# Kernel optimization log

Measured on AMD Instinct MI355X. Metric: run time of the kernel, lower is better.

Reference implementation:

```python
import jax, jax.numpy as jnp
import numpy as np

B, D_MODEL, N_LAYERS = 8, 512, 4
D_STATE, D_CONV, EXPAND, DT_RANK = 16, 4, 2, 32
D_INNER = EXPAND * D_MODEL
NUM_CLASSES = 10
ALPHA = 0.2  # observer_alpha
LN_EPS = 1e-5


def setup_inputs() -> dict:
    key = jax.random.key(0)
    ks = jax.random.split(key, 10)
    std = 0.02
    rn = lambda k, sh: (jax.random.normal(k, sh) * std).astype(jnp.float32)
    return {
        "x": jax.random.normal(ks[0], (B, 3, 32, 32), dtype=jnp.float32),
        "W_inp": rn(ks[1], (3, D_MODEL)), "b_inp": jnp.zeros((D_MODEL,), jnp.float32),
        "W_in": rn(ks[2], (N_LAYERS, D_MODEL, 2 * D_INNER)), "b_in": jnp.zeros((N_LAYERS, 2 * D_INNER), jnp.float32),
        "conv_w": rn(ks[3], (N_LAYERS, D_INNER, D_CONV)), "conv_b": jnp.zeros((N_LAYERS, D_INNER), jnp.float32),
        "W_x": rn(ks[4], (N_LAYERS, D_INNER, DT_RANK + 2 * D_STATE)),
        "W_dt": rn(ks[5], (N_LAYERS, DT_RANK, D_INNER)), "b_dt": jnp.zeros((N_LAYERS, D_INNER), jnp.float32),
        "A_log": jnp.broadcast_to(jnp.log(jnp.arange(1, D_STATE + 1, dtype=jnp.float32)), (N_LAYERS, D_INNER, D_STATE)) + 0.0,
        "D_skip": jnp.ones((N_LAYERS, D_INNER), jnp.float32),
        "W_out": rn(ks[6], (N_LAYERS, D_INNER, D_MODEL)), "b_out": jnp.zeros((N_LAYERS, D_MODEL), jnp.float32),
        "ln_w": jnp.ones((N_LAYERS, D_MODEL), jnp.float32), "ln_b": jnp.zeros((N_LAYERS, D_MODEL), jnp.float32),
        "lnf_w": jnp.ones((D_MODEL,), jnp.float32), "lnf_b": jnp.zeros((D_MODEL,), jnp.float32),
        "W_cls": rn(ks[7], (D_MODEL, NUM_CLASSES)), "b_cls": jnp.zeros((NUM_CLASSES,), jnp.float32),
    }


def layernorm(x, w, b):
    mu = x.mean(-1, keepdims=True)
    var = jnp.mean(jnp.square(x - mu), -1, keepdims=True)
    return (x - mu) * jax.lax.rsqrt(var + LN_EPS) * w + b


def mamba_layer(x, Wi, bi, cw, cb, Wx, Wdt, bdt, Alog, Dv, Wo, bo):
    # x: [B, L, d_model]
    Bsz, L, _ = x.shape
    u, z = jnp.split(x @ Wi + bi, 2, axis=-1)  # each [B, L, d_inner]
    # causal depthwise conv1d, kernel width D_CONV
    up = jnp.pad(u, ((0, 0), (D_CONV - 1, 0), (0, 0)))
    uc = cb + sum(up[:, k:k + L, :] * cw[:, k] for k in range(D_CONV))
    uc = jax.nn.silu(uc)
    dbc = uc @ Wx  # [B, L, dt_rank + 2*d_state]
    dt = jax.nn.softplus(dbc[..., :DT_RANK] @ Wdt + bdt)       # [B, L, d_inner]
    Bm = dbc[..., DT_RANK:DT_RANK + D_STATE]                    # [B, L, d_state]
    Cm = dbc[..., DT_RANK + D_STATE:]                           # [B, L, d_state]
    A = -jnp.exp(Alog)                                          # [d_inner, d_state]

    def step(h, inp):
        u_t, dt_t, B_t, C_t = inp  # [B,E],[B,E],[B,N],[B,N]
        h = jnp.exp(dt_t[..., None] * A) * h + (dt_t * u_t)[..., None] * B_t[:, None, :]
        # Luenberger observer correction: h <- h + alpha * (u - C.h) * C^T
        err = u_t - jnp.einsum('ben,bn->be', h, C_t)
        h = h + ALPHA * err[..., None] * C_t[:, None, :]
        y = jnp.einsum('ben,bn->be', h, C_t)
        return h, y

    step = jax.checkpoint(step)
    h0 = jnp.zeros((Bsz, D_INNER, D_STATE), dtype=x.dtype)
    xs = (uc.transpose(1, 0, 2), dt.transpose(1, 0, 2), Bm.transpose(1, 0, 2), Cm.transpose(1, 0, 2))
    _, ys = jax.lax.scan(step, h0, xs)
    y = ys.transpose(1, 0, 2) + Dv * uc
    y = y * jax.nn.silu(z)
    return y @ Wo + bo


def reference(x, W_inp, b_inp, W_in, b_in, conv_w, conv_b, W_x, W_dt, b_dt, A_log, D_skip, W_out, b_out, ln_w, ln_b, lnf_w, lnf_b, W_cls, b_cls):
    Bsz = x.shape[0]
    t = x.transpose(0, 2, 3, 1).reshape(Bsz, -1, 3)  # [B, H*W, 3]
    t = t @ W_inp + b_inp                             # [B, L, d_model]
    for i in range(N_LAYERS):
        t = t + mamba_layer(layernorm(t, ln_w[i], ln_b[i]), W_in[i], b_in[i], conv_w[i], conv_b[i], W_x[i], W_dt[i], b_dt[i], A_log[i], D_skip[i], W_out[i], b_out[i])
    t = t.mean(axis=1)
    t = layernorm(t, lnf_w, lnf_b)
    return t @ W_cls + b_cls
```

## Files before the change

kernel.cpp:

```cpp
#include <hip/hip_runtime.h>
#include <hip/hip_bf16.h>
#include <math.h>

#define BSZ 8
#define SEQL 1024
#define DM 512
#define DI 1024
#define DST 16
#define DTR 32
#define NLAYERS 4
#define ALPHA_C 0.2f
#define LNEPS 1e-5f
#define CH 64
#define KS64 8
#define YSTR 18

typedef __attribute__((ext_vector_type(8))) short short8;
typedef __attribute__((ext_vector_type(4))) float f32x4;

__device__ __forceinline__ void gll16(const void* g, void* l) {
    __builtin_amdgcn_global_load_lds(
        (const __attribute__((address_space(1))) unsigned int*)g,
        (__attribute__((address_space(3))) unsigned int*)l, 16, 0, 0);
}

__device__ __forceinline__ float sum16(float x) {
    x += __int_as_float(__builtin_amdgcn_update_dpp(0, __float_as_int(x), 0x121, 0xf, 0xf, true));
    x += __int_as_float(__builtin_amdgcn_update_dpp(0, __float_as_int(x), 0x122, 0xf, 0xf, true));
    x += __int_as_float(__builtin_amdgcn_update_dpp(0, __float_as_int(x), 0x124, 0xf, 0xf, true));
    x += __int_as_float(__builtin_amdgcn_update_dpp(0, __float_as_int(x), 0x128, 0xf, 0xf, true));
    return x;
}

__device__ __forceinline__ float bf2f(unsigned short v) {
    return __uint_as_float(((unsigned)v) << 16);
}

__global__ __launch_bounds__(256) void embed_kernel(const float* __restrict__ x,
                                                    const float* __restrict__ Wi,
                                                    const float* __restrict__ bi,
                                                    float* __restrict__ t) {
    int idx = blockIdx.x * 256 + threadIdx.x;
    if (idx >= BSZ * SEQL * DM) return;
    int d  = idx & (DM - 1);
    int bl = idx >> 9;
    int l  = bl & (SEQL - 1);
    int b  = bl >> 10;
    const float* xb = x + (size_t)b * 3 * SEQL;
    float acc = bi[d];
    acc += xb[0 * SEQL + l] * Wi[0 * DM + d];
    acc += xb[1 * SEQL + l] * Wi[1 * DM + d];
    acc += xb[2 * SEQL + l] * Wi[2 * DM + d];
    t[idx] = acc;
}

__global__ __launch_bounds__(256) void ln_kernel(const float* __restrict__ t,
                                                 const float* __restrict__ w,
                                                 const float* __restrict__ b,
                                                 __hip_bfloat16* __restrict__ xn) {
    int row = blockIdx.x;
    int tid = threadIdx.x;
    const float* r = t + (size_t)row * DM;
    float v0 = r[tid], v1 = r[tid + 256];
    __shared__ float sh[256], sh2[256];
    sh[tid]  = v0 + v1;
    sh2[tid] = v0 * v0 + v1 * v1;
    __syncthreads();
    for (int off = 128; off > 0; off >>= 1) {
        if (tid < off) { sh[tid] += sh[tid + off]; sh2[tid] += sh2[tid + off]; }
        __syncthreads();
    }
    float mu  = sh[0]  * (1.f / DM);
    float var = sh2[0] * (1.f / DM) - mu * mu;
    float rs  = rsqrtf(var + LNEPS);
    xn[(size_t)row * DM + tid]       = __float2bfloat16((v0 - mu) * rs * w[tid]       + b[tid]);
    xn[(size_t)row * DM + tid + 256] = __float2bfloat16((v1 - mu) * rs * w[tid + 256] + b[tid + 256]);
}

__global__ __launch_bounds__(256) void transpose_bf_kernel(const float* __restrict__ W,
                                                           __hip_bfloat16* __restrict__ Wt,
                                                           int K, int N, size_t lstride) {
    const float* Wl = W + (size_t)blockIdx.z * lstride;
    __hip_bfloat16* Wtl = Wt + (size_t)blockIdx.z * lstride;
    __shared__ float tile[32][33];
    int kk = blockIdx.x * 32, nn = blockIdx.y * 32;
    int tx = threadIdx.x & 31, ty = threadIdx.x >> 5;
#pragma unroll
    for (int i = 0; i < 32; i += 8)
        tile[ty + i][tx] = Wl[(size_t)(kk + ty + i) * N + nn + tx];
    __syncthreads();
#pragma unroll
    for (int i = 0; i < 32; i += 8)
        Wtl[(size_t)(nn + ty + i) * K + kk + tx] = __float2bfloat16(tile[tx][ty + i]);
}

template <int OUTMODE>
__global__ __launch_bounds__(256) void gemm_mfma_kernel(const short* __restrict__ A,
                                                        const short* __restrict__ Bt,
                                                        const float* __restrict__ bias,
                                                        void* __restrict__ Cv,
                                                        int M, int N, int K) {
    __shared__ __align__(16) short As[128 * 32];
    __shared__ __align__(16) short Bs[128 * 32];
    int tid = threadIdx.x;
    int w = tid >> 6, lane = tid & 63;
    int quad = lane >> 4, ml = lane & 15;
    int wm = w & 1, wn = w >> 1;
    const short* Ab = A + (size_t)blockIdx.x * 128 * K;
    const short* Bb = Bt + (size_t)blockIdx.y * 128 * K;
    f32x4 acc[4][4] = {};
    int s0 = tid, s1 = tid + 256;
    int r0 = s0 >> 2, c0 = (s0 & 3) ^ ((r0 >> 1) & 3);
    int r1 = s1 >> 2, c1 = (s1 & 3) ^ ((r1 >> 1) & 3);
    int aoff[4], boff[4];
#pragma unroll
    for (int t = 0; t < 4; t++) {
        int ra = wm * 64 + t * 16 + ml;
        aoff[t] = ra * 32 + (quad ^ ((ra >> 1) & 3)) * 8;
        int rb = wn * 64 + t * 16 + ml;
        boff[t] = rb * 32 + (quad ^ ((rb >> 1) & 3)) * 8;
    }
    for (int kk = 0; kk < K; kk += 32) {
        gll16(Ab + (size_t)r0 * K + kk + c0 * 8, As + (size_t)(w * 64) * 8);
        gll16(Ab + (size_t)r1 * K + kk + c1 * 8, As + (size_t)(256 + w * 64) * 8);
        gll16(Bb + (size_t)r0 * K + kk + c0 * 8, Bs + (size_t)(w * 64) * 8);
        gll16(Bb + (size_t)r1 * K + kk + c1 * 8, Bs + (size_t)(256 + w * 64) * 8);
        __syncthreads();
        short8 af[4], bfr[4];
#pragma unroll
        for (int t = 0; t < 4; t++) af[t]  = *(const short8*)&As[aoff[t]];
#pragma unroll
        for (int t = 0; t < 4; t++) bfr[t] = *(const short8*)&Bs[boff[t]];
#pragma unroll
        for (int mt = 0; mt < 4; mt++)
#pragma unroll
            for (int nt = 0; nt < 4; nt++)
                acc[mt][nt] = __builtin_amdgcn_mfma_f32_16x16x32_bf16(af[mt], bfr[nt], acc[mt][nt], 0, 0, 0);
        __syncthreads();
    }
#pragma unroll
    for (int mt = 0; mt < 4; mt++) {
#pragma unroll
        for (int nt = 0; nt < 4; nt++) {
            int n = blockIdx.y * 128 + wn * 64 + nt * 16 + ml;
            float bv = bias[n];
#pragma unroll
            for (int r = 0; r < 4; r++) {
                int m = blockIdx.x * 128 + wm * 64 + mt * 16 + quad * 4 + r;
                size_t off = (size_t)m * N + n;
                float v = acc[mt][nt][r] + bv;
                if (OUTMODE == 2) {
                    ((unsigned short*)Cv)[off] = __bfloat16_as_ushort(__float2bfloat16(v));
                } else {
                    float* C = (float*)Cv;
                    if (OUTMODE == 1) v += C[off];
                    C[off] = v;
                }
            }
        }
    }
}

__global__ __launch_bounds__(256) void gemm6464_res_kernel(const short* __restrict__ A,
                                                           const short* __restrict__ Bt,
                                                           const float* __restrict__ bias,
                                                           float* __restrict__ C,
                                                           int M, int N, int K) {
    __shared__ __align__(16) short As[64 * 32];
    __shared__ __align__(16) short Bs[64 * 32];
    int tid = threadIdx.x;
    int w = tid >> 6, lane = tid & 63;
    int quad = lane >> 4, ml = lane & 15;
    int wm = w & 1, wn = w >> 1;
    const short* Ab = A + (size_t)blockIdx.x * 64 * K;
    const short* Bb = Bt + (size_t)blockIdx.y * 64 * K;
    f32x4 acc[2][2] = {};
    int r0 = tid >> 2, c0 = (tid & 3) ^ ((r0 >> 1) & 3);
    int aoff[2], boff[2];
#pragma unroll
    for (int t = 0; t < 2; t++) {
        int ra = wm * 32 + t * 16 + ml;
        aoff[t] = ra * 32 + (quad ^ ((ra >> 1) & 3)) * 8;
        int rb = wn * 32 + t * 16 + ml;
        boff[t] = rb * 32 + (quad ^ ((rb >> 1) & 3)) * 8;
    }
    for (int kk = 0; kk < K; kk += 32) {
        gll16(Ab + (size_t)r0 * K + kk + c0 * 8, As + (size_t)(w * 64) * 8);
        gll16(Bb + (size_t)r0 * K + kk + c0 * 8, Bs + (size_t)(w * 64) * 8);
        __syncthreads();
        short8 af[2], bfr[2];
#pragma unroll
        for (int t = 0; t < 2; t++) af[t]  = *(const short8*)&As[aoff[t]];
#pragma unroll
        for (int t = 0; t < 2; t++) bfr[t] = *(const short8*)&Bs[boff[t]];
#pragma unroll
        for (int mt = 0; mt < 2; mt++)
#pragma unroll
            for (int nt = 0; nt < 2; nt++)
                acc[mt][nt] = __builtin_amdgcn_mfma_f32_16x16x32_bf16(af[mt], bfr[nt], acc[mt][nt], 0, 0, 0);
        __syncthreads();
    }
#pragma unroll
    for (int mt = 0; mt < 2; mt++) {
#pragma unroll
        for (int nt = 0; nt < 2; nt++) {
            int n = blockIdx.y * 64 + wn * 32 + nt * 16 + ml;
            float bv = bias[n];
#pragma unroll
            for (int r = 0; r < 4; r++) {
                int m = blockIdx.x * 64 + wm * 32 + mt * 16 + quad * 4 + r;
                size_t off = (size_t)m * N + n;
                C[off] = acc[mt][nt][r] + bv + C[off];
            }
        }
    }
}

__global__ __launch_bounds__(256) void conv_kernel(const unsigned short* __restrict__ uzb,
                                                   const float* __restrict__ cw,
                                                   const float* __restrict__ cb,
                                                   unsigned short* __restrict__ ucb) {
    int idx = blockIdx.x * 256 + threadIdx.x;
    int e  = idx & (DI - 1);
    int bl = idx >> 10;
    int l  = bl & (SEQL - 1);
    int b  = bl >> 10;
    const unsigned short* u = uzb + (size_t)b * SEQL * 2048;
    float acc = cb[e];
#pragma unroll
    for (int k = 0; k < 4; k++) {
        int ll = l - 3 + k;
        float uv = (ll >= 0) ? bf2f(u[(size_t)ll * 2048 + e]) : 0.f;
        acc += uv * cw[e * 4 + k];
    }
    acc = acc / (1.f + __expf(-acc));
    ucb[idx] = __bfloat16_as_ushort(__float2bfloat16(acc));
}

__global__ __launch_bounds__(256) void gemm64_mfma_kernel(const short* __restrict__ A,
                                                          const short* __restrict__ Bt,
                                                          float* __restrict__ part,
                                                          int M) {
    const int K = DI;
    const int Kseg = K / KS64;
    __shared__ __align__(16) short As[128 * 32];
    __shared__ __align__(16) short Bs[64 * 32];
    int tid = threadIdx.x;
    int w = tid >> 6, lane = tid & 63;
    int quad = lane >> 4, ml = lane & 15;
    int wm = w & 1, wn = w >> 1;
    int bm = blockIdx.x, ks = blockIdx.y;
    const short* Ab = A + (size_t)bm * 128 * K;
    f32x4 acc[4][2] = {};
    int s0 = tid, s1 = tid + 256;
    int r0 = s0 >> 2, c0 = (s0 & 3) ^ ((r0 >> 1) & 3);
    int r1 = s1 >> 2, c1 = (s1 & 3) ^ ((r1 >> 1) & 3);
    int rB = tid >> 2, cB = (tid & 3) ^ ((rB >> 1) & 3);
    int aoff[4], boff[2];
#pragma unroll
    for (int t = 0; t < 4; t++) {
        int ra = wm * 64 + t * 16 + ml;
        aoff[t] = ra * 32 + (quad ^ ((ra >> 1) & 3)) * 8;
    }
#pragma unroll
    for (int t = 0; t < 2; t++) {
        int rb = wn * 32 + t * 16 + ml;
        boff[t] = rb * 32 + (quad ^ ((rb >> 1) & 3)) * 8;
    }
    int k0 = ks * Kseg;
    for (int kk = k0; kk < k0 + Kseg; kk += 32) {
        gll16(Ab + (size_t)r0 * K + kk + c0 * 8, As + (size_t)(w * 64) * 8);
        gll16(Ab + (size_t)r1 * K + kk + c1 * 8, As + (size_t)(256 + w * 64) * 8);
        gll16(Bt + (size_t)rB * K + kk + cB * 8, Bs + (size_t)(w * 64) * 8);
        __syncthreads();
        short8 af[4], bfr[2];
#pragma unroll
        for (int t = 0; t < 4; t++) af[t]  = *(const short8*)&As[aoff[t]];
#pragma unroll
        for (int t = 0; t < 2; t++) bfr[t] = *(const short8*)&Bs[boff[t]];
#pragma unroll
        for (int mt = 0; mt < 4; mt++)
#pragma unroll
            for (int nt = 0; nt < 2; nt++)
                acc[mt][nt] = __builtin_amdgcn_mfma_f32_16x16x32_bf16(af[mt], bfr[nt], acc[mt][nt], 0, 0, 0);
        __syncthreads();
    }
#pragma unroll
    for (int mt = 0; mt < 4; mt++) {
#pragma unroll
        for (int nt = 0; nt < 2; nt++) {
            int n = wn * 32 + nt * 16 + ml;
#pragma unroll
            for (int r = 0; r < 4; r++) {
                int m = bm * 128 + wm * 64 + mt * 16 + quad * 4 + r;
                part[((size_t)ks * M + m) * 64 + n] = acc[mt][nt][r];
            }
        }
    }
}

__global__ __launch_bounds__(256) void repack_kernel(const float* __restrict__ part,
                                                     unsigned* __restrict__ bcb,
                                                     float* __restrict__ ssqb,
                                                     int M) {
    int m = blockIdx.x * 8 + (threadIdx.x >> 5);
    int j = threadIdx.x & 31;
    float v = 0.f;
#pragma unroll
    for (int ks = 0; ks < KS64; ks++) v += part[((size_t)ks * M + m) * 64 + 32 + j];
    int n = j & 15;
    unsigned short u16 = __bfloat16_as_ushort(__float2bfloat16(v));
    unsigned short* bp = (unsigned short*)(bcb + (size_t)m * 16 + n);
    if (j < 16) {
        bp[0] = u16;
    } else {
        bp[1] = u16;
        float vr = bf2f(u16);
        float s = sum16(vr * vr);
        if (j == 16) ssqb[m] = s;
    }
}

__global__ __launch_bounds__(256) void dt_kernel(const float* __restrict__ part,
                                                 const float* __restrict__ Wdt,
                                                 const float* __restrict__ bdt,
                                                 const unsigned short* __restrict__ ucb,
                                                 unsigned* __restrict__ dub,
                                                 int M) {
    __shared__ float sdtc[32][32];
    __shared__ float swdt[32][256];
    int tid = threadIdx.x;
    int e0 = (blockIdx.x & 3) * 256;
    int m0 = (blockIdx.x >> 2) * 32;
#pragma unroll
    for (int i = 0; i < 4; i++) {
        int idx = tid + 256 * i;
        int m = idx >> 5, r = idx & 31;
        float v = 0.f;
#pragma unroll
        for (int ks = 0; ks < KS64; ks++) v += part[((size_t)ks * M + m0 + m) * 64 + r];
        sdtc[m][r] = v;
    }
#pragma unroll
    for (int r = 0; r < 32; r++) swdt[r][tid] = Wdt[(size_t)r * DI + e0 + tid];
    __syncthreads();
    float wc[32];
#pragma unroll
    for (int r = 0; r < 32; r++) wc[r] = swdt[r][tid];
    float bv = bdt[e0 + tid];
    for (int m = 0; m < 32; m++) {
        float acc = bv;
#pragma unroll
        for (int r4 = 0; r4 < 8; r4++) {
            float4 d4 = *(const float4*)&sdtc[m][r4 * 4];
            acc = fmaf(d4.x, wc[r4 * 4 + 0], acc);
            acc = fmaf(d4.y, wc[r4 * 4 + 1], acc);
            acc = fmaf(d4.z, wc[r4 * 4 + 2], acc);
            acc = fmaf(d4.w, wc[r4 * 4 + 3], acc);
        }
        float sp = (acc > 20.f) ? acc : log1pf(__expf(acc));
        unsigned dt16 = (unsigned)__bfloat16_as_ushort(__float2bfloat16(sp));
        unsigned u16  = (unsigned)ucb[(size_t)(m0 + m) * DI + e0 + tid];
        dub[(size_t)(m0 + m) * DI + e0 + tid] = (dt16 << 16) | u16;
    }
}

__device__ __forceinline__ void scan_stage(unsigned* sDU, unsigned* sBC,
                                           const unsigned* __restrict__ dub_row,
                                           const unsigned* __restrict__ bcb_row,
                                           int e_base, int tid, int tc) {
    int w = tid >> 6;
    int t4 = tid >> 2, c4 = tid & 3;
    gll16(dub_row + (size_t)(tc + t4) * 1024 + e_base + c4 * 4, sDU + w * 256);
    gll16(bcb_row + (size_t)(tc + t4) * 16 + c4 * 4,            sBC + w * 256);
}

__device__ __forceinline__ void scan_flush(const float* yb, __hip_bfloat16* ob,
                                           int e_base, int tcp, int tid) {
#pragma unroll
    for (int r = 0; r < 2; r++) {
        int pid = r * 256 + tid;
        int t = pid >> 3, ep = pid & 7;
        float2 y2 = *(const float2*)&yb[t * YSTR + ep * 2];
        __hip_bfloat162 v;
        v.x = __float2bfloat16(y2.x);
        v.y = __float2bfloat16(y2.y);
        *(__hip_bfloat162*)&ob[(size_t)(tcp + t) * DI + e_base + ep * 2] = v;
    }
}

__global__ __launch_bounds__(256) void scan_kernel(const unsigned* __restrict__ dub,
                                                   const unsigned short* __restrict__ uzb,
                                                   const unsigned* __restrict__ bcb,
                                                   const float* __restrict__ ssqb,
                                                   const float* __restrict__ Alog,
                                                   const float* __restrict__ Dv,
                                                   __hip_bfloat16* __restrict__ out) {
    __shared__ __align__(16) unsigned sDU[2][CH * 16];
    __shared__ __align__(16) unsigned sBC[2][CH * 16];
    __shared__ __align__(16) float    yb [2][CH * YSTR];
    int tid = threadIdx.x;
    int g = tid >> 4, n = tid & 15;
    int b = blockIdx.x >> 6;
    int e_base = (blockIdx.x & 63) << 4;
    int e = e_base + g;
    float An2 = -__expf(Alog[e * DST + n]) * 1.4426950408889634f;
    float dv = Dv[e];
    const unsigned*       dub_row = dub + (size_t)b * SEQL * DI;
    const unsigned short* uzb_row = uzb + (size_t)b * SEQL * 2048;
    const unsigned*       bcb_row = bcb + (size_t)b * SEQL * 16;
    const float*          sqb     = ssqb + (size_t)b * SEQL;
    __hip_bfloat16* ob = out + (size_t)b * SEQL * DI;
    float h = 0.f;
    scan_stage(sDU[0], sBC[0], dub_row, bcb_row, e_base, tid, 0);
    int buf = 0;
    for (int c = 0; c < SEQL / CH; c++) {
        int tc = c * CH;
        __syncthreads();
        if (c + 1 < SEQL / CH)
            scan_stage(sDU[buf ^ 1], sBC[buf ^ 1], dub_row, bcb_row, e_base, tid, tc + CH);
        if (c > 0)
            scan_flush(yb[buf ^ 1], ob, e_base, tc - CH, tid);
        const unsigned* pDU = sDU[buf];
        const unsigned* pBC = sBC[buf];
        float* pY = yb[buf];
        for (int ts = 0; ts < CH; ts += 16) {
            int tl = ts + n;
            float sq = sqb[tc + tl];
            float zv = bf2f(uzb_row[(size_t)(tc + tl) * 2048 + 1024 + e]);
            float pc = 0.f, ucap = 0.f;
#pragma unroll
            for (int j = 0; j < 16; j++) {
                int t = ts + j;
                unsigned du = pDU[t * 16 + g];
                float dtv = __uint_as_float(du & 0xFFFF0000u);
                float uv  = __uint_as_float(du << 16);
                unsigned bcd = pBC[t * 16 + n];
                float Bn = __uint_as_float(bcd << 16);
                float Cn = __uint_as_float(bcd & 0xFFFF0000u);
                float a = __builtin_amdgcn_exp2f(dtv * An2);
                h = fmaf(a, h, dtv * uv * Bn);
                float p = sum16(h * Cn);
                h = fmaf(uv - p, ALPHA_C * Cn, h);
                bool cap = (n == j);
                pc   = cap ? p  : pc;
                ucap = cap ? uv : ucap;
            }
            float es2 = ALPHA_C * (ucap - pc);
            float y = fmaf(dv, ucap, fmaf(es2, sq, pc));
            float sz = zv / (1.f + __expf(-zv));
            pY[tl * YSTR + g] = y * sz;
        }
        buf ^= 1;
    }
    __syncthreads();
    scan_flush(yb[buf ^ 1], ob, e_base, SEQL - CH, tid);
}

__global__ __launch_bounds__(512) void pool_kernel(const float* __restrict__ t,
                                                   float* __restrict__ part) {
    int b = blockIdx.x >> 4;
    int c = blockIdx.x & 15;
    int d = threadIdx.x;
    const float* tb = t + ((size_t)b * SEQL + c * 64) * DM + d;
    float s = 0.f;
    for (int l = 0; l < 64; l++) s += tb[(size_t)l * DM];
    part[(size_t)blockIdx.x * DM + d] = s;
}

__global__ __launch_bounds__(512) void final_kernel(const float* __restrict__ part,
                                                    const float* __restrict__ lw,
                                                    const float* __restrict__ lb,
                                                    const float* __restrict__ Wc,
                                                    const float* __restrict__ bc,
                                                    float* __restrict__ out) {
    int b = blockIdx.x;
    int d = threadIdx.x;
    float v = 0.f;
    for (int c = 0; c < 16; c++) v += part[((size_t)b * 16 + c) * DM + d];
    v *= (1.f / SEQL);
    __shared__ float sh[512], sh2[512], nd[512];
    sh[d] = v; sh2[d] = v * v;
    __syncthreads();
    for (int off = 256; off > 0; off >>= 1) {
        if (d < off) { sh[d] += sh[d + off]; sh2[d] += sh2[d + off]; }
        __syncthreads();
    }
    float mu  = sh[0]  * (1.f / DM);
    float var = sh2[0] * (1.f / DM) - mu * mu;
    float rs  = rsqrtf(var + LNEPS);
    nd[d] = (v - mu) * rs * lw[d] + lb[d];
    __syncthreads();
    if (d < 10) {
        float acc = bc[d];
        for (int k = 0; k < DM; k++) acc += nd[k] * Wc[k * 10 + d];
        out[b * 10 + d] = acc;
    }
}

extern "C" void kernel_launch(void* const* d_in, const int* in_sizes, int n_in,
                              void* d_out, int out_size, void* d_ws, size_t ws_size,
                              hipStream_t stream) {
    const float* x      = (const float*)d_in[0];
    const float* W_inp  = (const float*)d_in[1];
    const float* b_inp  = (const float*)d_in[2];
    const float* W_in   = (const float*)d_in[3];
    const float* b_in   = (const float*)d_in[4];
    const float* conv_w = (const float*)d_in[5];
    const float* conv_b = (const float*)d_in[6];
    const float* W_x    = (const float*)d_in[7];
    const float* W_dt   = (const float*)d_in[8];
    const float* b_dt   = (const float*)d_in[9];
    const float* A_log  = (const float*)d_in[10];
    const float* D_skip = (const float*)d_in[11];
    const float* W_out  = (const float*)d_in[12];
    const float* b_out  = (const float*)d_in[13];
    const float* ln_w   = (const float*)d_in[14];
    const float* ln_b   = (const float*)d_in[15];
    const float* lnf_w  = (const float*)d_in[16];
    const float* lnf_b  = (const float*)d_in[17];
    const float* W_cls  = (const float*)d_in[18];
    const float* b_cls  = (const float*)d_in[19];

    const int M = BSZ * SEQL;

    float* ws = (float*)d_ws;
    float* t_buf = ws;                          ws += (size_t)M * DM;
    unsigned short* uzb = (unsigned short*)ws;  ws += (size_t)M * 2048 / 2;
    unsigned short* ucb = (unsigned short*)ws;  ws += (size_t)M * DI / 2;
    unsigned* dub  = (unsigned*)ws;             ws += (size_t)M * DI;
    unsigned* bcbu = (unsigned*)ws;             ws += (size_t)M * 16;
    float* ssqb  = ws;                          ws += (size_t)M;
    unsigned short* xn_bf = (unsigned short*)ws;  ws += (size_t)M * DM / 2;
    unsigned short* ucs_bf = (unsigned short*)ws; ws += (size_t)M * DI / 2;
    float* partb = ws;                          ws += (size_t)KS64 * M * 64;
    unsigned short* wtin_bf  = (unsigned short*)ws; ws += (size_t)NLAYERS * DM * 2048 / 2;
    unsigned short* wtout_bf = (unsigned short*)ws; ws += (size_t)NLAYERS * DI * DM / 2;
    unsigned short* wxt_bf   = (unsigned short*)ws; ws += (size_t)NLAYERS * DI * 64 / 2 + 64;
    float* poolp = ws;                          ws += (size_t)128 * DM;

    embed_kernel<<<(M * DM + 255) / 256, 256, 0, stream>>>(x, W_inp, b_inp, t_buf);
    transpose_bf_kernel<<<dim3(DM / 32, 2048 / 32, NLAYERS), 256, 0, stream>>>(
        W_in, (__hip_bfloat16*)wtin_bf, DM, 2048, (size_t)DM * 2048);
    transpose_bf_kernel<<<dim3(DI / 32, DM / 32, NLAYERS), 256, 0, stream>>>(
        W_out, (__hip_bfloat16*)wtout_bf, DI, DM, (size_t)DI * DM);
    transpose_bf_kernel<<<dim3(DI / 32, 64 / 32, NLAYERS), 256, 0, stream>>>(
        W_x, (__hip_bfloat16*)wxt_bf, DI, 64, (size_t)DI * 64);

    for (int i = 0; i < NLAYERS; i++) {
        ln_kernel<<<M, 256, 0, stream>>>(t_buf, ln_w + i * DM, ln_b + i * DM,
                                         (__hip_bfloat16*)xn_bf);
        gemm_mfma_kernel<2><<<dim3(M / 128, 2048 / 128), 256, 0, stream>>>(
            (const short*)xn_bf, (const short*)(wtin_bf + (size_t)i * DM * 2048),
            b_in + i * 2048, uzb, M, 2048, DM);
        conv_kernel<<<(M * DI) / 256, 256, 0, stream>>>(
            uzb, conv_w + (size_t)i * DI * 4, conv_b + i * DI, ucb);
        gemm64_mfma_kernel<<<dim3(M / 128, KS64), 256, 0, stream>>>(
            (const short*)ucb, (const short*)(wxt_bf + (size_t)i * DI * 64), partb, M);
        repack_kernel<<<M / 8, 256, 0, stream>>>(partb, bcbu, ssqb, M);
        dt_kernel<<<(M / 32) * 4, 256, 0, stream>>>(
            partb, W_dt + (size_t)i * DTR * DI, b_dt + i * DI, ucb, dub, M);
        scan_kernel<<<BSZ * DI / 16, 256, 0, stream>>>(
            dub, uzb, bcbu, ssqb, A_log + (size_t)i * DI * DST, D_skip + i * DI,
            (__hip_bfloat16*)ucs_bf);
        gemm6464_res_kernel<<<dim3(M / 64, DM / 64), 256, 0, stream>>>(
            (const short*)ucs_bf, (const short*)(wtout_bf + (size_t)i * DI * DM),
            b_out + i * DM, t_buf, M, DM, DI);
    }

    pool_kernel<<<128, 512, 0, stream>>>(t_buf, poolp);
    final_kernel<<<8, 512, 0, stream>>>(poolp, lnf_w, lnf_b, W_cls, b_cls, (float*)d_out);
}
```

Measured before the change: 1.164 ms.

## Stream scan inputs through register double-buffers instead of LDS staging

The selective-scan kernel stops staging the dt/u and B/C streams into shared memory with async global-to-LDS copies. Each thread now loads its own per-timestep values straight from global memory into two register arrays, prefetching the next 16 timesteps while it computes the current 16. This removes the LDS round trip and one barrier per chunk, keeping only the output staging buffer. The kernel also asks for two blocks per CU through launch bounds. In exchange, the 16 lanes sharing a channel make redundant global loads of the same value, and register pressure rises, which could cap occupancy or cause spills.

```diff
diff --git a/kernel.cpp b/kernel.cpp
--- a/kernel.cpp
+++ b/kernel.cpp
@@ -365,16 +365,6 @@
     }
 }
 
-__device__ __forceinline__ void scan_stage(unsigned* sDU, unsigned* sBC,
-                                           const unsigned* __restrict__ dub_row,
-                                           const unsigned* __restrict__ bcb_row,
-                                           int e_base, int tid, int tc) {
-    int w = tid >> 6;
-    int t4 = tid >> 2, c4 = tid & 3;
-    gll16(dub_row + (size_t)(tc + t4) * 1024 + e_base + c4 * 4, sDU + w * 256);
-    gll16(bcb_row + (size_t)(tc + t4) * 16 + c4 * 4,            sBC + w * 256);
-}
-
 __device__ __forceinline__ void scan_flush(const float* yb, __hip_bfloat16* ob,
                                            int e_base, int tcp, int tid) {
 #pragma unroll
@@ -389,16 +379,14 @@
     }
 }
 
-__global__ __launch_bounds__(256) void scan_kernel(const unsigned* __restrict__ dub,
-                                                   const unsigned short* __restrict__ uzb,
-                                                   const unsigned* __restrict__ bcb,
-                                                   const float* __restrict__ ssqb,
-                                                   const float* __restrict__ Alog,
-                                                   const float* __restrict__ Dv,
-                                                   __hip_bfloat16* __restrict__ out) {
-    __shared__ __align__(16) unsigned sDU[2][CH * 16];
-    __shared__ __align__(16) unsigned sBC[2][CH * 16];
-    __shared__ __align__(16) float    yb [2][CH * YSTR];
+__global__ __launch_bounds__(256, 2) void scan_kernel(const unsigned* __restrict__ dub,
+                                                      const unsigned short* __restrict__ uzb,
+                                                      const unsigned* __restrict__ bcb,
+                                                      const float* __restrict__ ssqb,
+                                                      const float* __restrict__ Alog,
+                                                      const float* __restrict__ Dv,
+                                                      __hip_bfloat16* __restrict__ out) {
+    __shared__ __align__(16) float yb[2][CH * YSTR];
     int tid = threadIdx.x;
     int g = tid >> 4, n = tid & 15;
     int b = blockIdx.x >> 6;
@@ -406,55 +394,69 @@
     int e = e_base + g;
     float An2 = -__expf(Alog[e * DST + n]) * 1.4426950408889634f;
     float dv = Dv[e];
-    const unsigned*       dub_row = dub + (size_t)b * SEQL * DI;
-    const unsigned short* uzb_row = uzb + (size_t)b * SEQL * 2048;
-    const unsigned*       bcb_row = bcb + (size_t)b * SEQL * 16;
-    const float*          sqb     = ssqb + (size_t)b * SEQL;
+    const unsigned*       duP = dub + (size_t)b * SEQL * DI + e;
+    const unsigned short* zP  = uzb + (size_t)b * SEQL * 2048 + 1024 + e;
+    const unsigned*       bcP = bcb + (size_t)b * SEQL * 16 + n;
+    const float*          sqP = ssqb + (size_t)b * SEQL;
     __hip_bfloat16* ob = out + (size_t)b * SEQL * DI;
     float h = 0.f;
-    scan_stage(sDU[0], sBC[0], dub_row, bcb_row, e_base, tid, 0);
-    int buf = 0;
+    unsigned duA[16], bcA[16], duB[16], bcB[16];
+#pragma unroll
+    for (int j = 0; j < 16; j++) { duA[j] = duP[(size_t)j * DI]; bcA[j] = bcP[j * 16]; }
+
+#define LOADG(DU, BC, TS)                                                        \
+    if ((TS) < SEQL) {                                                           \
+        _Pragma("unroll")                                                        \
+        for (int j = 0; j < 16; j++) {                                           \
+            DU[j] = duP[(size_t)((TS) + j) * DI];                                \
+            BC[j] = bcP[((TS) + j) * 16];                                        \
+        }                                                                        \
+    }
+
+#define PROCESS(DU, BC, TS, PY)                                                  \
+    {                                                                            \
+        int tl = ((TS) & (CH - 1)) + n;                                          \
+        float sq = sqP[(TS) + n];                                                \
+        float zv = bf2f(zP[(size_t)((TS) + n) * 2048]);                          \
+        float pc = 0.f, ucap = 0.f;                                              \
+        _Pragma("unroll")                                                        \
+        for (int j = 0; j < 16; j++) {                                           \
+            unsigned du = DU[j];                                                 \
+            float dtv = __uint_as_float(du & 0xFFFF0000u);                       \
+            float uv  = __uint_as_float(du << 16);                               \
+            unsigned bcd = BC[j];                                                \
+            float Bn = __uint_as_float(bcd << 16);                               \
+            float Cn = __uint_as_float(bcd & 0xFFFF0000u);                       \
+            float a = __builtin_amdgcn_exp2f(dtv * An2);                         \
+            h = fmaf(a, h, dtv * uv * Bn);                                       \
+            float p = sum16(h * Cn);                                             \
+            h = fmaf(uv - p, ALPHA_C * Cn, h);                                   \
+            bool cap = (n == j);                                                 \
+            pc   = cap ? p  : pc;                                                \
+            ucap = cap ? uv : ucap;                                              \
+        }                                                                        \
+        float es2 = ALPHA_C * (ucap - pc);                                       \
+        float y = fmaf(dv, ucap, fmaf(es2, sq, pc));                             \
+        float sz = zv / (1.f + __expf(-zv));                                     \
+        PY[tl * YSTR + g] = y * sz;                                              \
+    }
+
     for (int c = 0; c < SEQL / CH; c++) {
-        int tc = c * CH;
-        __syncthreads();
-        if (c + 1 < SEQL / CH)
-            scan_stage(sDU[buf ^ 1], sBC[buf ^ 1], dub_row, bcb_row, e_base, tid, tc + CH);
-        if (c > 0)
-            scan_flush(yb[buf ^ 1], ob, e_base, tc - CH, tid);
-        const unsigned* pDU = sDU[buf];
-        const unsigned* pBC = sBC[buf];
-        float* pY = yb[buf];
-        for (int ts = 0; ts < CH; ts += 16) {
-            int tl = ts + n;
-            float sq = sqb[tc + tl];
-            float zv = bf2f(uzb_row[(size_t)(tc + tl) * 2048 + 1024 + e]);
-            float pc = 0.f, ucap = 0.f;
-#pragma unroll
-            for (int j = 0; j < 16; j++) {
-                int t = ts + j;
-                unsigned du = pDU[t * 16 + g];
-                float dtv = __uint_as_float(du & 0xFFFF0000u);
-                float uv  = __uint_as_float(du << 16);
-                unsigned bcd = pBC[t * 16 + n];
-                float Bn = __uint_as_float(bcd << 16);
-                float Cn = __uint_as_float(bcd & 0xFFFF0000u);
-                float a = __builtin_amdgcn_exp2f(dtv * An2);
-                h = fmaf(a, h, dtv * uv * Bn);
-                float p = sum16(h * Cn);
-                h = fmaf(uv - p, ALPHA_C * Cn, h);
-                bool cap = (n == j);
-                pc   = cap ? p  : pc;
-                ucap = cap ? uv : ucap;
-            }
-            float es2 = ALPHA_C * (ucap - pc);
-            float y = fmaf(dv, ucap, fmaf(es2, sq, pc));
-            float sz = zv / (1.f + __expf(-zv));
-            pY[tl * YSTR + g] = y * sz;
-        }
-        buf ^= 1;
-    }
-    __syncthreads();
-    scan_flush(yb[buf ^ 1], ob, e_base, SEQL - CH, tid);
+        float* pY = yb[c & 1];
+        int t0 = c * CH;
+        LOADG(duB, bcB, t0 + 16);
+        PROCESS(duA, bcA, t0, pY);
+        LOADG(duA, bcA, t0 + 32);
+        PROCESS(duB, bcB, t0 + 16, pY);
+        LOADG(duB, bcB, t0 + 48);
+        PROCESS(duA, bcA, t0 + 32, pY);
+        LOADG(duA, bcA, t0 + 64);
+        PROCESS(duB, bcB, t0 + 48, pY);
+        __syncthreads();
+        scan_flush(pY, ob, e_base, t0, tid);
+    }
+#undef LOADG
+#undef PROCESS
 }
 
 __global__ __launch_bounds__(512) void pool_kernel(const float* __restrict__ t,
```

Measured after the change: 1.232 ms. +5.9%, slower.
